# Kernel tuning notes

Hardware: AMD Instinct MI355X
Metric: run time of the kernel (lower is better)

The kernel has to match this reference:

```python
import jax, jax.numpy as jnp
import numpy as np

N_HEADS = 8
N_NODES = 100_000
DEG = 16
N_EDGES = N_NODES * DEG
IN_DIM = 256
OUT_DIM = 128


def setup_inputs() -> dict:
    key = jax.random.key(0)
    k1, k2, k3, k4 = jax.random.split(key, 4)
    X = jax.random.normal(k1, (N_NODES, IN_DIM), dtype=jnp.float32)
    weights = jax.random.normal(k2, (IN_DIM, OUT_DIM), dtype=jnp.float32) * (1.0 / np.sqrt(IN_DIM))
    attention_w = jax.random.normal(k3, (1, N_HEADS), dtype=jnp.float32) * 0.1
    # valid CSR with uniform degree DEG
    row_pointers = (jnp.arange(N_NODES + 1, dtype=jnp.int32) * DEG)
    column_index = jax.random.randint(k4, (N_EDGES,), 0, N_NODES, dtype=jnp.int32)
    # TC-GNN block bookkeeping tensors: kernel-schedule metadata, no effect on math
    blockPartition = jnp.zeros(((N_NODES + 15) // 16,), dtype=jnp.int32)
    edgeToColumn = jnp.zeros((N_EDGES,), dtype=jnp.int32)
    edgeToRow = jnp.zeros((N_EDGES,), dtype=jnp.int32)
    return {
        "X": X,
        "weights": weights,
        "attention_w": attention_w,
        "row_pointers": row_pointers,
        "column_index": column_index,
        "blockPartition": blockPartition,
        "edgeToColumn": edgeToColumn,
        "edgeToRow": edgeToRow,
    }


def reference(X, weights, attention_w, row_pointers, column_index,
              blockPartition, edgeToColumn, edgeToRow):
    n_nodes = X.shape[0]
    n_edges = column_index.shape[0]
    # dense projection: X_prime = X @ W  -> [n_nodes, out_dim]
    X_prime = X @ weights
    # CSR row id of each edge: row_ids[e] = r s.t. row_pointers[r] <= e < row_pointers[r+1]
    row_ids = jnp.searchsorted(row_pointers,
                               jnp.arange(n_edges, dtype=row_pointers.dtype),
                               side="right") - 1
    # SDDMM (GAcc.forward_ef): per-edge scalar feature = <X_prime[src], X_prime[dst]>
    dst = X_prime[column_index]                    # [E, out_dim]
    edge_feature = jnp.sum(X_prime[row_ids] * dst, axis=-1)  # [E]
    # edge_attentions = outer(edge_feature, attention_w) -> [n_heads, E];
    # aggregation kernel collapses heads: att_e = edge_feature_e * sum_h(w_h)
    att = edge_feature * jnp.sum(attention_w)      # [E]
    # attention-weighted SpMM (GAcc.forward_gat): scatter-add into destination rows
    out = jax.ops.segment_sum(att[:, None] * dst, row_ids, num_segments=n_nodes)
    return out
```

## Files before the change

### kernel.cpp

```cpp
#include <hip/hip_runtime.h>
#include <hip/hip_bf16.h>
#include <stdint.h>

#define N_NODES 100000
#define IN_DIM 256
#define OUT_DIM 128
#define DEG 16

typedef __bf16 bf16x8 __attribute__((ext_vector_type(8)));
typedef __bf16 bf16x4 __attribute__((ext_vector_type(4)));
typedef float f32x4 __attribute__((ext_vector_type(4)));

__global__ void prep_w_kernel(const float* __restrict__ W, __bf16* __restrict__ Wt) {
    const int j = blockIdx.x;
    const int k = threadIdx.x;
    Wt[j * IN_DIM + k] = (__bf16)W[k * OUT_DIM + j];
}

__global__ __launch_bounds__(256) void gemm_kernel(const float* __restrict__ X,
                                                   const __bf16* __restrict__ Wt,
                                                   __bf16* __restrict__ XP) {
    __shared__ __bf16 Alds[64][264];
    const int t = threadIdx.x;
    const int m0 = blockIdx.x * 64;

    #pragma unroll
    for (int i = 0; i < 16; ++i) {
        const int flat = i * 256 + t;
        const int row  = flat >> 6;
        const int col  = (flat & 63) * 4;
        int grow = m0 + row;
        if (grow >= N_NODES) grow = N_NODES - 1;
        float4 v = *reinterpret_cast<const float4*>(X + (size_t)grow * IN_DIM + col);
        bf16x4 b;
        b[0] = (__bf16)v.x; b[1] = (__bf16)v.y; b[2] = (__bf16)v.z; b[3] = (__bf16)v.w;
        *reinterpret_cast<bf16x4*>(&Alds[row][col]) = b;
    }
    __syncthreads();

    const int lane = t & 63;
    const int wave = t >> 6;
    const int n0 = wave * 32;
    const int lr = lane & 15;
    const int lg = lane >> 4;

    f32x4 acc[4][2] = {};
    const __bf16* bp0 = Wt + (size_t)(n0 + lr) * IN_DIM + lg * 8;
    const __bf16* bp1 = bp0 + 16 * IN_DIM;

    #pragma unroll
    for (int ks = 0; ks < 8; ++ks) {
        const int ko = ks * 32 + lg * 8;
        bf16x8 b0 = *reinterpret_cast<const bf16x8*>(bp0 + ks * 32);
        bf16x8 b1 = *reinterpret_cast<const bf16x8*>(bp1 + ks * 32);
        bf16x8 a[4];
        #pragma unroll
        for (int mi = 0; mi < 4; ++mi)
            a[mi] = *reinterpret_cast<const bf16x8*>(&Alds[mi * 16 + lr][ko]);
        #pragma unroll
        for (int mi = 0; mi < 4; ++mi) {
            acc[mi][0] = __builtin_amdgcn_mfma_f32_16x16x32_bf16(a[mi], b0, acc[mi][0], 0, 0, 0);
            acc[mi][1] = __builtin_amdgcn_mfma_f32_16x16x32_bf16(a[mi], b1, acc[mi][1], 0, 0, 0);
        }
    }

    #pragma unroll
    for (int mi = 0; mi < 4; ++mi)
        #pragma unroll
        for (int ni = 0; ni < 2; ++ni)
            #pragma unroll
            for (int r = 0; r < 4; ++r) {
                const int row = m0 + mi * 16 + lg * 4 + r;
                if (row < N_NODES) {
                    const int col = n0 + ni * 16 + lr;
                    XP[(size_t)row * OUT_DIM + col] = (__bf16)acc[mi][ni][r];
                }
            }
}

__global__ __launch_bounds__(256) void gat_edge_kernel(const __bf16* __restrict__ XP,
                                                       const int* __restrict__ rp,
                                                       const int* __restrict__ ci,
                                                       const float* __restrict__ attw,
                                                       float* __restrict__ out) {
    const int lane = threadIdx.x & 63;
    const int row = blockIdx.x * 4 + (threadIdx.x >> 6);
    const int g = lane >> 4;
    const int sl = lane & 15;

    float s = 0.f;
    #pragma unroll
    for (int h = 0; h < 8; ++h) s += attw[h];

    float x[8];
    {
        uint4 xv = *reinterpret_cast<const uint4*>(XP + (size_t)row * OUT_DIM + sl * 8);
        const uint32_t* xw = reinterpret_cast<const uint32_t*>(&xv);
        #pragma unroll
        for (int i = 0; i < 4; ++i) {
            x[2 * i]     = __uint_as_float(xw[i] << 16);
            x[2 * i + 1] = __uint_as_float(xw[i] & 0xffff0000u);
        }
    }

    const int4 cv = reinterpret_cast<const int4*>(ci + (size_t)row * DEG)[g];
    const int c[4] = {cv.x, cv.y, cv.z, cv.w};

    uint4 dvu[4];
    #pragma unroll
    for (int j = 0; j < 4; ++j)
        dvu[j] = *reinterpret_cast<const uint4*>(XP + (size_t)c[j] * OUT_DIM + sl * 8);

    float d[4][8];
    #pragma unroll
    for (int j = 0; j < 4; ++j) {
        const uint32_t* dw = reinterpret_cast<const uint32_t*>(&dvu[j]);
        #pragma unroll
        for (int i = 0; i < 4; ++i) {
            d[j][2 * i]     = __uint_as_float(dw[i] << 16);
            d[j][2 * i + 1] = __uint_as_float(dw[i] & 0xffff0000u);
        }
    }

    float p[4];
    #pragma unroll
    for (int j = 0; j < 4; ++j) {
        float t0 = 0.f;
        #pragma unroll
        for (int i = 0; i < 8; ++i) t0 += x[i] * d[j][i];
        p[j] = t0;
    }
    #pragma unroll
    for (int off = 1; off <= 8; off <<= 1) {
        #pragma unroll
        for (int j = 0; j < 4; ++j) p[j] += __shfl_xor(p[j], off);
    }

    float acc[8] = {};
    #pragma unroll
    for (int j = 0; j < 4; ++j) {
        const float att = p[j] * s;
        #pragma unroll
        for (int i = 0; i < 8; ++i) acc[i] += att * d[j][i];
    }

    #pragma unroll
    for (int off = 16; off <= 32; off <<= 1) {
        #pragma unroll
        for (int i = 0; i < 8; ++i) acc[i] += __shfl_xor(acc[i], off);
    }

    if (g == 0) {
        float4 o0, o1;
        o0.x = acc[0]; o0.y = acc[1]; o0.z = acc[2]; o0.w = acc[3];
        o1.x = acc[4]; o1.y = acc[5]; o1.z = acc[6]; o1.w = acc[7];
        float* dst = out + (size_t)row * OUT_DIM + sl * 8;
        *reinterpret_cast<float4*>(dst) = o0;
        *reinterpret_cast<float4*>(dst + 4) = o1;
    }
}

extern "C" void kernel_launch(void* const* d_in, const int* in_sizes, int n_in,
                              void* d_out, int out_size, void* d_ws, size_t ws_size,
                              hipStream_t stream) {
    const float* X    = (const float*)d_in[0];
    const float* W    = (const float*)d_in[1];
    const float* attw = (const float*)d_in[2];
    const int*   rp   = (const int*)d_in[3];
    const int*   ci   = (const int*)d_in[4];
    float* out = (float*)d_out;

    __bf16* XP = (__bf16*)d_ws;
    __bf16* Wt = (__bf16*)((char*)d_ws + (size_t)N_NODES * OUT_DIM * 2);

    prep_w_kernel<<<OUT_DIM, IN_DIM, 0, stream>>>(W, Wt);
    gemm_kernel<<<(N_NODES + 63) / 64, 256, 0, stream>>>(X, Wt, XP);
    gat_edge_kernel<<<N_NODES / 4, 256, 0, stream>>>(XP, rp, ci, attw, out);
}
```

Before: 97.42 us.

## Split GEMM K staging into halves and process two rows per wave in edge kernel

The GEMM now loads the second half of the X tile into shared memory before computing on the first half, aiming to overlap global loads with MFMA work. The edge kernel assigns two rows per wave and issues all neighbor gathers up front to raise memory-level parallelism. The weight-prep kernel is changed to read W in coalesced order. Costs are higher register pressure in the edge kernel and an extra barrier in the GEMM.

```diff
diff --git a/kernel.cpp b/kernel.cpp
--- a/kernel.cpp
+++ b/kernel.cpp
@@ -12,31 +12,18 @@
 typedef float f32x4 __attribute__((ext_vector_type(4)));
 
 __global__ void prep_w_kernel(const float* __restrict__ W, __bf16* __restrict__ Wt) {
-    const int j = blockIdx.x;
-    const int k = threadIdx.x;
-    Wt[j * IN_DIM + k] = (__bf16)W[k * OUT_DIM + j];
+    const int idx = blockIdx.x * 256 + threadIdx.x;
+    const int k = idx >> 7;
+    const int j = idx & 127;
+    Wt[j * IN_DIM + k] = (__bf16)W[idx];
 }
 
 __global__ __launch_bounds__(256) void gemm_kernel(const float* __restrict__ X,
                                                    const __bf16* __restrict__ Wt,
                                                    __bf16* __restrict__ XP) {
-    __shared__ __bf16 Alds[64][264];
+    __shared__ __bf16 Alds[2][64][136];
     const int t = threadIdx.x;
     const int m0 = blockIdx.x * 64;
-
-    #pragma unroll
-    for (int i = 0; i < 16; ++i) {
-        const int flat = i * 256 + t;
-        const int row  = flat >> 6;
-        const int col  = (flat & 63) * 4;
-        int grow = m0 + row;
-        if (grow >= N_NODES) grow = N_NODES - 1;
-        float4 v = *reinterpret_cast<const float4*>(X + (size_t)grow * IN_DIM + col);
-        bf16x4 b;
-        b[0] = (__bf16)v.x; b[1] = (__bf16)v.y; b[2] = (__bf16)v.z; b[3] = (__bf16)v.w;
-        *reinterpret_cast<bf16x4*>(&Alds[row][col]) = b;
-    }
-    __syncthreads();
 
     const int lane = t & 63;
     const int wave = t >> 6;
@@ -44,25 +31,51 @@
     const int lr = lane & 15;
     const int lg = lane >> 4;
 
+    const int srow = (t >> 5) * 8;
+    const int scol = (t & 31) * 4;
+
+    auto stage = [&](int h) {
+        #pragma unroll
+        for (int i = 0; i < 8; ++i) {
+            const int row = i * 8 + (t >> 5);
+            int grow = m0 + row;
+            if (grow >= N_NODES) grow = N_NODES - 1;
+            float4 v = *reinterpret_cast<const float4*>(
+                X + (size_t)grow * IN_DIM + h * 128 + scol);
+            bf16x4 b;
+            b[0] = (__bf16)v.x; b[1] = (__bf16)v.y; b[2] = (__bf16)v.z; b[3] = (__bf16)v.w;
+            *reinterpret_cast<bf16x4*>(&Alds[h][row][scol]) = b;
+        }
+    };
+
     f32x4 acc[4][2] = {};
     const __bf16* bp0 = Wt + (size_t)(n0 + lr) * IN_DIM + lg * 8;
     const __bf16* bp1 = bp0 + 16 * IN_DIM;
 
-    #pragma unroll
-    for (int ks = 0; ks < 8; ++ks) {
-        const int ko = ks * 32 + lg * 8;
-        bf16x8 b0 = *reinterpret_cast<const bf16x8*>(bp0 + ks * 32);
-        bf16x8 b1 = *reinterpret_cast<const bf16x8*>(bp1 + ks * 32);
-        bf16x8 a[4];
-        #pragma unroll
-        for (int mi = 0; mi < 4; ++mi)
-            a[mi] = *reinterpret_cast<const bf16x8*>(&Alds[mi * 16 + lr][ko]);
-        #pragma unroll
-        for (int mi = 0; mi < 4; ++mi) {
-            acc[mi][0] = __builtin_amdgcn_mfma_f32_16x16x32_bf16(a[mi], b0, acc[mi][0], 0, 0, 0);
-            acc[mi][1] = __builtin_amdgcn_mfma_f32_16x16x32_bf16(a[mi], b1, acc[mi][1], 0, 0, 0);
-        }
-    }
+    auto compute_half = [&](int h) {
+        #pragma unroll
+        for (int ks = 0; ks < 4; ++ks) {
+            const int ko = ks * 32 + lg * 8;
+            bf16x8 b0 = *reinterpret_cast<const bf16x8*>(bp0 + h * 128 + ks * 32);
+            bf16x8 b1 = *reinterpret_cast<const bf16x8*>(bp1 + h * 128 + ks * 32);
+            bf16x8 a[4];
+            #pragma unroll
+            for (int mi = 0; mi < 4; ++mi)
+                a[mi] = *reinterpret_cast<const bf16x8*>(&Alds[h][mi * 16 + lr][ko]);
+            #pragma unroll
+            for (int mi = 0; mi < 4; ++mi) {
+                acc[mi][0] = __builtin_amdgcn_mfma_f32_16x16x32_bf16(a[mi], b0, acc[mi][0], 0, 0, 0);
+                acc[mi][1] = __builtin_amdgcn_mfma_f32_16x16x32_bf16(a[mi], b1, acc[mi][1], 0, 0, 0);
+            }
+        }
+    };
+
+    stage(0);
+    __syncthreads();
+    stage(1);
+    compute_half(0);
+    __syncthreads();
+    compute_half(1);
 
     #pragma unroll
     for (int mi = 0; mi < 4; ++mi)
@@ -84,7 +97,9 @@
                                                        const float* __restrict__ attw,
                                                        float* __restrict__ out) {
     const int lane = threadIdx.x & 63;
-    const int row = blockIdx.x * 4 + (threadIdx.x >> 6);
+    const int wave = threadIdx.x >> 6;
+    const int rowA = blockIdx.x * 8 + wave * 2;
+    const int rowB = rowA + 1;
     const int g = lane >> 4;
     const int sl = lane & 15;
 
@@ -92,71 +107,126 @@
     #pragma unroll
     for (int h = 0; h < 8; ++h) s += attw[h];
 
-    float x[8];
+    const int4 cvA = reinterpret_cast<const int4*>(ci + (size_t)rowA * DEG)[g];
+    const int4 cvB = reinterpret_cast<const int4*>(ci + (size_t)rowB * DEG)[g];
+    const uint4 xvA = *reinterpret_cast<const uint4*>(XP + (size_t)rowA * OUT_DIM + sl * 8);
+    const uint4 xvB = *reinterpret_cast<const uint4*>(XP + (size_t)rowB * OUT_DIM + sl * 8);
+
+    const int cA[4] = {cvA.x, cvA.y, cvA.z, cvA.w};
+    const int cB[4] = {cvB.x, cvB.y, cvB.z, cvB.w};
+
+    uint4 dvA[4], dvB[4];
+    #pragma unroll
+    for (int j = 0; j < 4; ++j)
+        dvA[j] = *reinterpret_cast<const uint4*>(XP + (size_t)cA[j] * OUT_DIM + sl * 8);
+    #pragma unroll
+    for (int j = 0; j < 4; ++j)
+        dvB[j] = *reinterpret_cast<const uint4*>(XP + (size_t)cB[j] * OUT_DIM + sl * 8);
+
     {
-        uint4 xv = *reinterpret_cast<const uint4*>(XP + (size_t)row * OUT_DIM + sl * 8);
-        const uint32_t* xw = reinterpret_cast<const uint32_t*>(&xv);
+        float x[8];
+        const uint32_t* xw = reinterpret_cast<const uint32_t*>(&xvA);
         #pragma unroll
         for (int i = 0; i < 4; ++i) {
             x[2 * i]     = __uint_as_float(xw[i] << 16);
             x[2 * i + 1] = __uint_as_float(xw[i] & 0xffff0000u);
         }
+        float d[4][8];
+        #pragma unroll
+        for (int j = 0; j < 4; ++j) {
+            const uint32_t* dw = reinterpret_cast<const uint32_t*>(&dvA[j]);
+            #pragma unroll
+            for (int i = 0; i < 4; ++i) {
+                d[j][2 * i]     = __uint_as_float(dw[i] << 16);
+                d[j][2 * i + 1] = __uint_as_float(dw[i] & 0xffff0000u);
+            }
+        }
+        float p[4];
+        #pragma unroll
+        for (int j = 0; j < 4; ++j) {
+            float t0 = 0.f;
+            #pragma unroll
+            for (int i = 0; i < 8; ++i) t0 += x[i] * d[j][i];
+            p[j] = t0;
+        }
+        #pragma unroll
+        for (int off = 1; off <= 8; off <<= 1) {
+            #pragma unroll
+            for (int j = 0; j < 4; ++j) p[j] += __shfl_xor(p[j], off);
+        }
+        float acc[8] = {};
+        #pragma unroll
+        for (int j = 0; j < 4; ++j) {
+            const float att = p[j] * s;
+            #pragma unroll
+            for (int i = 0; i < 8; ++i) acc[i] += att * d[j][i];
+        }
+        #pragma unroll
+        for (int off = 16; off <= 32; off <<= 1) {
+            #pragma unroll
+            for (int i = 0; i < 8; ++i) acc[i] += __shfl_xor(acc[i], off);
+        }
+        if (g == 0) {
+            float4 o0, o1;
+            o0.x = acc[0]; o0.y = acc[1]; o0.z = acc[2]; o0.w = acc[3];
+            o1.x = acc[4]; o1.y = acc[5]; o1.z = acc[6]; o1.w = acc[7];
+            float* dst = out + (size_t)rowA * OUT_DIM + sl * 8;
+            *reinterpret_cast<float4*>(dst) = o0;
+            *reinterpret_cast<float4*>(dst + 4) = o1;
+        }
     }
 
-    const int4 cv = reinterpret_cast<const int4*>(ci + (size_t)row * DEG)[g];
-    const int c[4] = {cv.x, cv.y, cv.z, cv.w};
-
-    uint4 dvu[4];
-    #pragma unroll
-    for (int j = 0; j < 4; ++j)
-        dvu[j] = *reinterpret_cast<const uint4*>(XP + (size_t)c[j] * OUT_DIM + sl * 8);
-
-    float d[4][8];
-    #pragma unroll
-    for (int j = 0; j < 4; ++j) {
-        const uint32_t* dw = reinterpret_cast<const uint32_t*>(&dvu[j]);
+    {
+        float x[8];
+        const uint32_t* xw = reinterpret_cast<const uint32_t*>(&xvB);
         #pragma unroll
         for (int i = 0; i < 4; ++i) {
-            d[j][2 * i]     = __uint_as_float(dw[i] << 16);
-            d[j][2 * i + 1] = __uint_as_float(dw[i] & 0xffff0000u);
-        }
-    }
-
-    float p[4];
-    #pragma unroll
-    for (int j = 0; j < 4; ++j) {
-        float t0 = 0.f;
-        #pragma unroll
-        for (int i = 0; i < 8; ++i) t0 += x[i] * d[j][i];
-        p[j] = t0;
-    }
-    #pragma unroll
-    for (int off = 1; off <= 8; off <<= 1) {
-        #pragma unroll
-        for (int j = 0; j < 4; ++j) p[j] += __shfl_xor(p[j], off);
-    }
-
-    float acc[8] = {};
-    #pragma unroll
-    for (int j = 0; j < 4; ++j) {
-        const float att = p[j] * s;
-        #pragma unroll
-        for (int i = 0; i < 8; ++i) acc[i] += att * d[j][i];
-    }
-
-    #pragma unroll
-    for (int off = 16; off <= 32; off <<= 1) {
-        #pragma unroll
-        for (int i = 0; i < 8; ++i) acc[i] += __shfl_xor(acc[i], off);
-    }
-
-    if (g == 0) {
-        float4 o0, o1;
-        o0.x = acc[0]; o0.y = acc[1]; o0.z = acc[2]; o0.w = acc[3];
-        o1.x = acc[4]; o1.y = acc[5]; o1.z = acc[6]; o1.w = acc[7];
-        float* dst = out + (size_t)row * OUT_DIM + sl * 8;
-        *reinterpret_cast<float4*>(dst) = o0;
-        *reinterpret_cast<float4*>(dst + 4) = o1;
+            x[2 * i]     = __uint_as_float(xw[i] << 16);
+            x[2 * i + 1] = __uint_as_float(xw[i] & 0xffff0000u);
+        }
+        float d[4][8];
+        #pragma unroll
+        for (int j = 0; j < 4; ++j) {
+            const uint32_t* dw = reinterpret_cast<const uint32_t*>(&dvB[j]);
+            #pragma unroll
+            for (int i = 0; i < 4; ++i) {
+                d[j][2 * i]     = __uint_as_float(dw[i] << 16);
+                d[j][2 * i + 1] = __uint_as_float(dw[i] & 0xffff0000u);
+            }
+        }
+        float p[4];
+        #pragma unroll
+        for (int j = 0; j < 4; ++j) {
+            float t0 = 0.f;
+            #pragma unroll
+            for (int i = 0; i < 8; ++i) t0 += x[i] * d[j][i];
+            p[j] = t0;
+        }
+        #pragma unroll
+        for (int off = 1; off <= 8; off <<= 1) {
+            #pragma unroll
+            for (int j = 0; j < 4; ++j) p[j] += __shfl_xor(p[j], off);
+        }
+        float acc[8] = {};
+        #pragma unroll
+        for (int j = 0; j < 4; ++j) {
+            const float att = p[j] * s;
+            #pragma unroll
+            for (int i = 0; i < 8; ++i) acc[i] += att * d[j][i];
+        }
+        #pragma unroll
+        for (int off = 16; off <= 32; off <<= 1) {
+            #pragma unroll
+            for (int i = 0; i < 8; ++i) acc[i] += __shfl_xor(acc[i], off);
+        }
+        if (g == 0) {
+            float4 o0, o1;
+            o0.x = acc[0]; o0.y = acc[1]; o0.z = acc[2]; o0.w = acc[3];
+            o1.x = acc[4]; o1.y = acc[5]; o1.z = acc[6]; o1.w = acc[7];
+            float* dst = out + (size_t)rowB * OUT_DIM + sl * 8;
+            *reinterpret_cast<float4*>(dst) = o0;
+            *reinterpret_cast<float4*>(dst + 4) = o1;
+        }
     }
 }
 
@@ -173,7 +243,7 @@
     __bf16* XP = (__bf16*)d_ws;
     __bf16* Wt = (__bf16*)((char*)d_ws + (size_t)N_NODES * OUT_DIM * 2);
 
-    prep_w_kernel<<<OUT_DIM, IN_DIM, 0, stream>>>(W, Wt);
+    prep_w_kernel<<<(IN_DIM * OUT_DIM) / 256, 256, 0, stream>>>(W, Wt);
     gemm_kernel<<<(N_NODES + 63) / 64, 256, 0, stream>>>(X, Wt, XP);
-    gat_edge_kernel<<<N_NODES / 4, 256, 0, stream>>>(XP, rp, ci, attw, out);
-}
+    gat_edge_kernel<<<N_NODES / 8, 256, 0, stream>>>(XP, rp, ci, attw, out);
+}
```

After: 98.16 us. No clear change (+0.8%).
